# Performance work log

Measured on AMD Instinct MI355X. Metric: run time of the kernel, lower is better.

Reference implementation:

```python
import jax, jax.numpy as jnp
import numpy as np

B, T, C, H = 4, 2048, 1024, 16
DK = C // H


def setup_inputs() -> dict:
    key = jax.random.key(0)
    ks = jax.random.split(key, 12)
    s = 1.0 / np.sqrt(C)
    return {
        "q": jax.random.normal(ks[0], (B, T, C), jnp.float32),
        "k": jax.random.normal(ks[1], (B, T, C), jnp.float32),
        "v": jax.random.normal(ks[2], (B, T, C), jnp.float32),
        "mask": jax.random.randint(ks[3], (B, T, T), 0, 2, jnp.int32),
        "Wq": jax.random.normal(ks[4], (C, C), jnp.float32) * s,
        "bq": jnp.zeros((C,), jnp.float32),
        "Wk": jax.random.normal(ks[5], (C, C), jnp.float32) * s,
        "bk": jnp.zeros((C,), jnp.float32),
        "Wv": jax.random.normal(ks[6], (C, C), jnp.float32) * s,
        "bv": jnp.zeros((C,), jnp.float32),
        "Wf": jax.random.normal(ks[7], (C, C), jnp.float32) * s,
        "bf": jnp.zeros((C,), jnp.float32),
    }


def reference(q, k, v, mask, Wq, bq, Wk, bk, Wv, bv, Wf, bf):
    # linear projections (torch Linear: x @ W.T + b), then split heads
    def heads(x, W, b):
        y = x @ W.T + b  # [B,T,C]
        return y.reshape(B, T, H, DK).transpose(0, 2, 1, 3)  # [B,H,T,DK]

    qh, kh, vh = heads(q, Wq, bq), heads(k, Wk, bk), heads(v, Wv, bv)
    att = jnp.einsum("bhqd,bhkd->bhqk", qh, kh) * (1.0 / np.sqrt(DK))
    att = jnp.where(mask[:, None, :, :] == 0, jnp.float32(-1e9), att)
    p = jax.nn.softmax(att, axis=-1)
    y = jnp.einsum("bhqk,bhkd->bhqd", p, vh)  # [B,H,T,DK]
    y = y.transpose(0, 2, 1, 3).reshape(B, T, C)
    return y @ Wf.T + bf
```

## Files before the change

kernel.cpp:

```cpp
#include <hip/hip_runtime.h>

#define B_ 4
#define T_ 2048
#define C_ 1024
#define H_ 16
#define DK_ 64
#define BT_ 8192

using u16 = unsigned short;
using u32 = unsigned int;
using u64 = unsigned long long;
typedef __attribute__((ext_vector_type(8))) short short8;
typedef __attribute__((ext_vector_type(4))) float f32x4;
typedef __attribute__((ext_vector_type(16))) float f32x16;
typedef __attribute__((ext_vector_type(4))) u32 u32x4;
typedef __attribute__((ext_vector_type(2))) u32 u32x2;

__device__ __forceinline__ u16 f2bf(float f) {
  u32 u = __builtin_bit_cast(u32, f);
  u32 r = u + 0x7fffu + ((u >> 16) & 1u);
  return (u16)(r >> 16);
}

__device__ __forceinline__ void glds16(void* lds, const void* g) {
  __builtin_amdgcn_global_load_lds(
      (__attribute__((address_space(1))) u32*)g,
      (__attribute__((address_space(3))) u32*)lds, 16, 0, 0);
}

__device__ __forceinline__ u32 cvtpk_bf16(float lo, float hi) {
  u32 r;
  asm("v_cvt_pk_bf16_f32 %0, %1, %2" : "=v"(r) : "v"(lo), "v"(hi));
  return r;
}

__device__ __forceinline__ void cvt_range(const float* __restrict__ s,
                                          u16* __restrict__ d, int n,
                                          int rb, int nblk) {
  int i0 = (rb * 256 + (int)threadIdx.x) * 4;
  int stride = nblk * 256 * 4;
  for (int i = i0; i < n; i += stride) {
    float4 v = *(const float4*)(s + i);
    u64 p = (u64)f2bf(v.x) | ((u64)f2bf(v.y) << 16) |
            ((u64)f2bf(v.z) << 32) | ((u64)f2bf(v.w) << 48);
    *(u64*)(d + i) = p;
  }
}

__global__ __launch_bounds__(256) void prep_k(
    const float* __restrict__ q, const float* __restrict__ k,
    const float* __restrict__ v, const float* __restrict__ Wq,
    const float* __restrict__ Wk, const float* __restrict__ Wv,
    const float* __restrict__ Wf, const int* __restrict__ mask,
    u16* __restrict__ qb, u16* __restrict__ kb, u16* __restrict__ vb,
    u16* __restrict__ Wqb, u16* __restrict__ Wkb, u16* __restrict__ Wvb,
    u16* __restrict__ Wfb, u64* __restrict__ mb) {
  const int bid = blockIdx.x;
  if (bid < 1260) {
    const int which = bid / 420, rb = bid % 420;
    const float* s = which == 0 ? q : which == 1 ? k : v;
    u16* d = which == 0 ? qb : which == 1 ? kb : vb;
    cvt_range(s, d, BT_ * C_, rb, 420);
  } else if (bid < 1468) {
    const int which = (bid - 1260) / 52, rb = (bid - 1260) % 52;
    const float* s = which == 0 ? Wq : which == 1 ? Wk : which == 2 ? Wv : Wf;
    u16* d = which == 0 ? Wqb : which == 1 ? Wkb : which == 2 ? Wvb : Wfb;
    cvt_range(s, d, C_ * C_, rb, 52);
  } else {
    const int nch = B_ * T_ * T_ / 256;
    const int lane = threadIdx.x & 63;
    int g0 = (bid - 1468) * 16 + ((int)threadIdx.x >> 6) * 4;
    for (int g = g0; g < nch; g += 580 * 16) {
#pragma unroll
      for (int gg = 0; gg < 4; ++gg) {
        const int4 vv = *(const int4*)(mask + (size_t)(g + gg) * 256 + 4 * lane);
        const u64 b0 = __ballot(vv.x != 0);
        const u64 b1 = __ballot(vv.y != 0);
        const u64 b2 = __ballot(vv.z != 0);
        const u64 b3 = __ballot(vv.w != 0);
        const u64 wv = lane == 0 ? b0 : lane == 1 ? b1 : lane == 2 ? b2 : b3;
        if (lane < 4) mb[(size_t)(g + gg) * 4 + lane] = wv;
      }
    }
  }
}

template <int MODE>
__global__ __launch_bounds__(256) void gemm_nt(
    const u16* __restrict__ A, const u16* __restrict__ Bmat,
    const float* __restrict__ bias, void* __restrict__ out,
    int M, int N, int K, float scale) {
  __shared__ __align__(16) u16 As[128 * 32];
  __shared__ __align__(16) u16 Bs[128 * 32];
  const int t = threadIdx.x;
  const int lane = t & 63;
  const int wave = t >> 6;
  const int wr = wave >> 1, wc = wave & 1;
  const int lr = lane & 15, lg = lane >> 4;
  const int m0 = blockIdx.x * 128;
  const int n0 = blockIdx.y * 128;

  f32x4 acc[4][4] = {};

  const int srow = t >> 2;
  const int scol = (t & 3) * 8;
  const u16* ag = A + (size_t)(m0 + srow) * K + scol;
  const u16* bg = Bmat + (size_t)(n0 + srow) * K + scol;
  u16* as0 = &As[srow * 32 + scol];
  u16* as1 = &As[(srow + 64) * 32 + scol];
  u16* bs0 = &Bs[srow * 32 + scol];
  u16* bs1 = &Bs[(srow + 64) * 32 + scol];

  for (int k0 = 0; k0 < K; k0 += 32) {
    glds16(as0, ag + k0);
    glds16(as1, ag + (size_t)64 * K + k0);
    glds16(bs0, bg + k0);
    glds16(bs1, bg + (size_t)64 * K + k0);
    __syncthreads();
    short8 af[4], bf[4];
#pragma unroll
    for (int m = 0; m < 4; ++m)
      af[m] = *(const short8*)&As[(wr * 64 + m * 16 + lr) * 32 + lg * 8];
#pragma unroll
    for (int n = 0; n < 4; ++n)
      bf[n] = *(const short8*)&Bs[(wc * 64 + n * 16 + lr) * 32 + lg * 8];
#pragma unroll
    for (int m = 0; m < 4; ++m)
#pragma unroll
      for (int n = 0; n < 4; ++n)
        acc[m][n] = __builtin_amdgcn_mfma_f32_16x16x32_bf16(af[m], bf[n], acc[m][n], 0, 0, 0);
    __syncthreads();
  }

#pragma unroll
  for (int m = 0; m < 4; ++m) {
#pragma unroll
    for (int n = 0; n < 4; ++n) {
#pragma unroll
      for (int j = 0; j < 4; ++j) {
        const int gm = m0 + wr * 64 + m * 16 + lg * 4 + j;
        const int gn = n0 + wc * 64 + n * 16 + lr;
        float v = acc[m][n][j];
        if (MODE == 0) {
          v = (v + bias[gn]) * scale;
          const int b = gm >> 11, tt = gm & 2047, h = gn >> 6, d = gn & 63;
          ((u16*)out)[((((size_t)b * H_ + h) * T_ + tt) << 6) + d] = f2bf(v);
        } else if (MODE == 1) {
          v += bias[gm];
          const int gnp = (gn & ~12) | ((gn & 4) << 1) | ((gn & 8) >> 1);
          ((u16*)out)[(size_t)gm * N + gnp] = f2bf(v);
        } else {
          v += bias[gn];
          ((float*)out)[(size_t)gm * N + gn] = v;
        }
      }
    }
  }
}

__global__ __launch_bounds__(512) void attn32_k(
    const u16* __restrict__ Qh, const u16* __restrict__ Kh,
    const u16* __restrict__ Vt, const u64* __restrict__ mb,
    u16* __restrict__ Y) {
  __shared__ __align__(16) u16 Ks[2][64 * 68];
  __shared__ __align__(16) u16 Vs[2][64 * 68];

  const int f = blockIdx.x;
  const int lgid = ((f & 7) << 6) | (f >> 3);
  const int bh = lgid >> 3, qblk = lgid & 7;
  const int b = bh >> 4, h = bh & 15;
  const int t = threadIdx.x;
  const int wave = t >> 6, lane = t & 63;
  const int lq = lane & 31, hi = lane >> 5;
  const int q0 = qblk * 256 + wave * 32;

  const u16* Qp = Qh + ((size_t)bh * T_ + q0 + lq) * DK_ + hi * 8;
  short8 qf[4];
#pragma unroll
  for (int kt = 0; kt < 4; ++kt) qf[kt] = *(const short8*)(Qp + kt * 16);

  const u16* KgB = Kh + (size_t)bh * T_ * DK_;
  const u16* VtB = Vt + (size_t)h * DK_ * BT_ + (size_t)b * T_;
  const u64* mrow = mb + ((size_t)b * T_ + q0 + lq) * (T_ / 64);

  const int sr = t >> 3, sj = t & 7;
  const u16* ksrc0 = KgB + (size_t)sr * DK_ + sj * 8;
  const u16* vsrc0 = VtB + (size_t)sr * BT_ + sj * 8;
  const int ldst = sr * 68 + sj * 8;

  const u32x4 onesu = {0x3F803F80u, 0x3F803F80u, 0x3F803F80u, 0x3F803F80u};
  const short8 ones8 = __builtin_bit_cast(short8, onesu);

  f32x16 o0 = {}, o1 = {}, accl = {};

  u32x4 kpre = *(const u32x4*)(ksrc0);
  u32x4 vpre = *(const u32x4*)(vsrc0);
  *(u32x2*)&Ks[0][ldst] = (u32x2){kpre[0], kpre[1]};
  *(u32x2*)&Ks[0][ldst + 4] = (u32x2){kpre[2], kpre[3]};
  *(u32x2*)&Vs[0][ldst] = (u32x2){vpre[0], vpre[1]};
  *(u32x2*)&Vs[0][ldst + 4] = (u32x2){vpre[2], vpre[3]};
  __syncthreads();
  int cur = 0;

  for (int kv = 0; kv < T_; kv += 64) {
    const bool pre = (kv + 64) < T_;
    if (pre) {
      kpre = *(const u32x4*)(ksrc0 + (size_t)(kv + 64) * DK_);
      vpre = *(const u32x4*)(vsrc0 + (kv + 64));
    }

    f32x16 c0 = {}, c1 = {};
    __builtin_amdgcn_s_setprio(1);
#pragma unroll
    for (int kt = 0; kt < 4; ++kt) {
      const int ix = (2 * kt + hi) * 8;
      const u32x2 a0 = *(const u32x2*)&Ks[cur][lq * 68 + ix];
      const u32x2 a1 = *(const u32x2*)&Ks[cur][lq * 68 + ix + 4];
      const u32x2 b0 = *(const u32x2*)&Ks[cur][(lq + 32) * 68 + ix];
      const u32x2 b1 = *(const u32x2*)&Ks[cur][(lq + 32) * 68 + ix + 4];
      const u32x4 k0u = {a0[0], a0[1], a1[0], a1[1]};
      const u32x4 k1u = {b0[0], b0[1], b1[0], b1[1]};
      c0 = __builtin_amdgcn_mfma_f32_32x32x16_bf16(
          __builtin_bit_cast(short8, k0u), qf[kt], c0, 0, 0, 0);
      c1 = __builtin_amdgcn_mfma_f32_32x32x16_bf16(
          __builtin_bit_cast(short8, k1u), qf[kt], c1, 0, 0, 0);
    }
    __builtin_amdgcn_s_setprio(0);

    const u64* wp = mrow + ((kv >> 8) << 2);
    const int sh = ((kv >> 2) & 48) + hi;
    u32 tp[4];
#pragma unroll
    for (int e = 0; e < 4; ++e) tp[e] = (u32)(wp[e] >> sh);
#pragma unroll
    for (int r = 0; r < 16; ++r) {
      const int pp = 2 * (r >> 2);
      const u32 k0m = (u32)(((int)(tp[r & 3] << (31 - pp))) >> 31);
      const u32 k1m = (u32)(((int)(tp[r & 3] << (23 - pp))) >> 31);
      c0[r] = __builtin_bit_cast(
          float, __builtin_bit_cast(u32, __builtin_amdgcn_exp2f(c0[r])) & k0m);
      c1[r] = __builtin_bit_cast(
          float, __builtin_bit_cast(u32, __builtin_amdgcn_exp2f(c1[r])) & k1m);
    }

    u32 pw_[4][4];
#pragma unroll
    for (int g = 0; g < 4; ++g) {
      const int ob = (g & 1) * 8;
#pragma unroll
      for (int w2 = 0; w2 < 4; ++w2) {
        const float lo = (g < 2) ? c0[ob + 2 * w2] : c1[ob + 2 * w2];
        const float hii = (g < 2) ? c0[ob + 2 * w2 + 1] : c1[ob + 2 * w2 + 1];
        pw_[g][w2] = cvtpk_bf16(lo, hii);
      }
    }

    __builtin_amdgcn_s_setprio(1);
#pragma unroll
    for (int g = 0; g < 4; ++g) {
      const int ix = (2 * g + hi) * 8;
      const u32x2 va = *(const u32x2*)&Vs[cur][lq * 68 + ix];
      const u32x2 vb = *(const u32x2*)&Vs[cur][lq * 68 + ix + 4];
      const u32x2 wa = *(const u32x2*)&Vs[cur][(lq + 32) * 68 + ix];
      const u32x2 wb = *(const u32x2*)&Vs[cur][(lq + 32) * 68 + ix + 4];
      const u32x4 pu = {pw_[g][0], pw_[g][1], pw_[g][2], pw_[g][3]};
      const u32x4 v0u = {va[0], va[1], vb[0], vb[1]};
      const u32x4 v1u = {wa[0], wa[1], wb[0], wb[1]};
      const short8 pa = __builtin_bit_cast(short8, pu);
      o0 = __builtin_amdgcn_mfma_f32_32x32x16_bf16(
          pa, __builtin_bit_cast(short8, v0u), o0, 0, 0, 0);
      o1 = __builtin_amdgcn_mfma_f32_32x32x16_bf16(
          pa, __builtin_bit_cast(short8, v1u), o1, 0, 0, 0);
      accl = __builtin_amdgcn_mfma_f32_32x32x16_bf16(pa, ones8, accl, 0, 0, 0);
    }
    __builtin_amdgcn_s_setprio(0);

    if (pre) {
      *(u32x2*)&Ks[cur ^ 1][ldst] = (u32x2){kpre[0], kpre[1]};
      *(u32x2*)&Ks[cur ^ 1][ldst + 4] = (u32x2){kpre[2], kpre[3]};
      *(u32x2*)&Vs[cur ^ 1][ldst] = (u32x2){vpre[0], vpre[1]};
      *(u32x2*)&Vs[cur ^ 1][ldst + 4] = (u32x2){vpre[2], vpre[3]};
    }
    __syncthreads();
    cur ^= 1;
  }

#pragma unroll
  for (int r = 0; r < 16; ++r) {
    const int row = (r & 3) + 8 * (r >> 2) + 4 * hi;
    const float li = 1.0f / accl[r];
    u16* yp = Y + ((size_t)b * T_ + q0 + row) * C_ + h * DK_ + lq;
    yp[0] = f2bf(o0[r] * li);
    yp[32] = f2bf(o1[r] * li);
  }
}

extern "C" void kernel_launch(void* const* d_in, const int* in_sizes, int n_in,
                              void* d_out, int out_size, void* d_ws, size_t ws_size,
                              hipStream_t stream) {
  const float* q  = (const float*)d_in[0];
  const float* k  = (const float*)d_in[1];
  const float* v  = (const float*)d_in[2];
  const int* mask = (const int*)d_in[3];
  const float* Wq = (const float*)d_in[4];
  const float* bq = (const float*)d_in[5];
  const float* Wk = (const float*)d_in[6];
  const float* bk = (const float*)d_in[7];
  const float* Wv = (const float*)d_in[8];
  const float* bv = (const float*)d_in[9];
  const float* Wf = (const float*)d_in[10];
  const float* bf = (const float*)d_in[11];
  float* out = (float*)d_out;
  char* ws = (char*)d_ws;

  size_t off = 0;
  auto nxt = [&](size_t bytes) -> void* {
    void* p = ws + off;
    off += (bytes + 255) & ~(size_t)255;
    return p;
  };
  const size_t big = (size_t)BT_ * C_ * 2;
  const size_t wsz = (size_t)C_ * C_ * 2;
  u16* qb  = (u16*)nxt(big);
  u16* kb  = (u16*)nxt(big);
  u16* vb  = (u16*)nxt(big);
  u16* Wqb = (u16*)nxt(wsz);
  u16* Wkb = (u16*)nxt(wsz);
  u16* Wvb = (u16*)nxt(wsz);
  u16* Wfb = (u16*)nxt(wsz);
  u16* Qh  = (u16*)nxt(big);
  u16* Kh  = (u16*)nxt(big);
  u16* Vt  = (u16*)nxt(big);
  u16* Yb  = (u16*)nxt(big);
  u64* mb  = (u64*)nxt((size_t)B_ * T_ * (T_ / 64) * 8);

  prep_k<<<2048, 256, 0, stream>>>(q, k, v, Wq, Wk, Wv, Wf, mask,
                                   qb, kb, vb, Wqb, Wkb, Wvb, Wfb, mb);

  const float qscale = 0.125f * 1.4426950408889634f;
  gemm_nt<0><<<dim3(BT_ / 128, C_ / 128), 256, 0, stream>>>(qb, Wqb, bq, Qh, BT_, C_, C_, qscale);
  gemm_nt<0><<<dim3(BT_ / 128, C_ / 128), 256, 0, stream>>>(kb, Wkb, bk, Kh, BT_, C_, C_, 1.0f);
  gemm_nt<1><<<dim3(C_ / 128, BT_ / 128), 256, 0, stream>>>(Wvb, vb, bv, Vt, C_, BT_, C_, 1.0f);

  attn32_k<<<B_ * H_ * (T_ / 256), 512, 0, stream>>>(Qh, Kh, Vt, mb, Yb);

  gemm_nt<2><<<dim3(BT_ / 128, C_ / 128), 256, 0, stream>>>(Yb, Wfb, bf, out, BT_, C_, C_, 1.0f);
}
```

Baseline: 266.7 us.

## Fuse fp32-to-bf16 activation conversion into projection GEMMs and widen attention KV tile

The separate prep pass that converted q, k and v to bf16 is removed. The projection GEMMs now load fp32 activations directly, convert them in registers and store bf16 into LDS, with a register prefetch one k-step ahead. The Q and K projections are batched into a single launch through blockIdx.z. The attention kernel now stages 128 keys per LDS buffer and processes them as two 64-key sub-steps, halving the number of barriers and global prefetch rounds at the cost of more LDS and registers. Folding the conversion into the GEMMs cuts a full write and reread of bf16 activations, but the fp32 A operand doubles the GEMM's global load bytes.

Result: slower. 278.1 us (+4.3%).

```diff
diff --git a/kernel.cpp b/kernel.cpp
--- a/kernel.cpp
+++ b/kernel.cpp
@@ -48,29 +48,22 @@
 }
 
 __global__ __launch_bounds__(256) void prep_k(
-    const float* __restrict__ q, const float* __restrict__ k,
-    const float* __restrict__ v, const float* __restrict__ Wq,
-    const float* __restrict__ Wk, const float* __restrict__ Wv,
-    const float* __restrict__ Wf, const int* __restrict__ mask,
-    u16* __restrict__ qb, u16* __restrict__ kb, u16* __restrict__ vb,
+    const float* __restrict__ Wq, const float* __restrict__ Wk,
+    const float* __restrict__ Wv, const float* __restrict__ Wf,
+    const int* __restrict__ mask,
     u16* __restrict__ Wqb, u16* __restrict__ Wkb, u16* __restrict__ Wvb,
     u16* __restrict__ Wfb, u64* __restrict__ mb) {
   const int bid = blockIdx.x;
-  if (bid < 1260) {
-    const int which = bid / 420, rb = bid % 420;
-    const float* s = which == 0 ? q : which == 1 ? k : v;
-    u16* d = which == 0 ? qb : which == 1 ? kb : vb;
-    cvt_range(s, d, BT_ * C_, rb, 420);
-  } else if (bid < 1468) {
-    const int which = (bid - 1260) / 52, rb = (bid - 1260) % 52;
+  if (bid < 256) {
+    const int which = bid >> 6, rb = bid & 63;
     const float* s = which == 0 ? Wq : which == 1 ? Wk : which == 2 ? Wv : Wf;
     u16* d = which == 0 ? Wqb : which == 1 ? Wkb : which == 2 ? Wvb : Wfb;
-    cvt_range(s, d, C_ * C_, rb, 52);
+    cvt_range(s, d, C_ * C_, rb, 64);
   } else {
     const int nch = B_ * T_ * T_ / 256;
     const int lane = threadIdx.x & 63;
-    int g0 = (bid - 1468) * 16 + ((int)threadIdx.x >> 6) * 4;
-    for (int g = g0; g < nch; g += 580 * 16) {
+    int g0 = (bid - 256) * 16 + ((int)threadIdx.x >> 6) * 4;
+    for (int g = g0; g < nch; g += 1792 * 16) {
 #pragma unroll
       for (int gg = 0; gg < 4; ++gg) {
         const int4 vv = *(const int4*)(mask + (size_t)(g + gg) * 256 + 4 * lane);
@@ -85,13 +78,21 @@
   }
 }
 
-template <int MODE>
+template <int MODE, int AF, int BF>
 __global__ __launch_bounds__(256) void gemm_nt(
-    const u16* __restrict__ A, const u16* __restrict__ Bmat,
-    const float* __restrict__ bias, void* __restrict__ out,
-    int M, int N, int K, float scale) {
+    const void* __restrict__ Aa, const void* __restrict__ Ab,
+    const void* __restrict__ Ba, const void* __restrict__ Bb,
+    const float* __restrict__ biasa, const float* __restrict__ biasb,
+    void* __restrict__ outa, void* __restrict__ outb,
+    int M, int N, int K, float scalea, float scaleb) {
   __shared__ __align__(16) u16 As[128 * 32];
   __shared__ __align__(16) u16 Bs[128 * 32];
+  const void* A = blockIdx.z ? Ab : Aa;
+  const void* Bm = blockIdx.z ? Bb : Ba;
+  const float* bias = blockIdx.z ? biasb : biasa;
+  void* out = blockIdx.z ? outb : outa;
+  const float scale = blockIdx.z ? scaleb : scalea;
+
   const int t = threadIdx.x;
   const int lane = t & 63;
   const int wave = t >> 6;
@@ -104,18 +105,65 @@
 
   const int srow = t >> 2;
   const int scol = (t & 3) * 8;
-  const u16* ag = A + (size_t)(m0 + srow) * K + scol;
-  const u16* bg = Bmat + (size_t)(n0 + srow) * K + scol;
   u16* as0 = &As[srow * 32 + scol];
   u16* as1 = &As[(srow + 64) * 32 + scol];
   u16* bs0 = &Bs[srow * 32 + scol];
   u16* bs1 = &Bs[(srow + 64) * 32 + scol];
 
+  const u16* ag = (const u16*)A + (size_t)(m0 + srow) * K + scol;
+  const float* agf = (const float*)A + (size_t)(m0 + srow) * K + scol;
+  const u16* bg = (const u16*)Bm + (size_t)(n0 + srow) * K + scol;
+  const float* bgf = (const float*)Bm + (size_t)(n0 + srow) * K + scol;
+
+  float4 ax0, ax1, ax2, ax3, bx0, bx1, bx2, bx3;
+  if (AF) {
+    ax0 = *(const float4*)(agf);
+    ax1 = *(const float4*)(agf + 4);
+    ax2 = *(const float4*)(agf + (size_t)64 * K);
+    ax3 = *(const float4*)(agf + (size_t)64 * K + 4);
+  }
+  if (BF) {
+    bx0 = *(const float4*)(bgf);
+    bx1 = *(const float4*)(bgf + 4);
+    bx2 = *(const float4*)(bgf + (size_t)64 * K);
+    bx3 = *(const float4*)(bgf + (size_t)64 * K + 4);
+  }
+
   for (int k0 = 0; k0 < K; k0 += 32) {
-    glds16(as0, ag + k0);
-    glds16(as1, ag + (size_t)64 * K + k0);
-    glds16(bs0, bg + k0);
-    glds16(bs1, bg + (size_t)64 * K + k0);
+    if (AF) {
+      const u32x4 p0 = {cvtpk_bf16(ax0.x, ax0.y), cvtpk_bf16(ax0.z, ax0.w),
+                        cvtpk_bf16(ax1.x, ax1.y), cvtpk_bf16(ax1.z, ax1.w)};
+      const u32x4 p1 = {cvtpk_bf16(ax2.x, ax2.y), cvtpk_bf16(ax2.z, ax2.w),
+                        cvtpk_bf16(ax3.x, ax3.y), cvtpk_bf16(ax3.z, ax3.w)};
+      *(u32x4*)as0 = p0;
+      *(u32x4*)as1 = p1;
+      if (k0 + 32 < K) {
+        ax0 = *(const float4*)(agf + k0 + 32);
+        ax1 = *(const float4*)(agf + k0 + 36);
+        ax2 = *(const float4*)(agf + (size_t)64 * K + k0 + 32);
+        ax3 = *(const float4*)(agf + (size_t)64 * K + k0 + 36);
+      }
+    } else {
+      glds16(as0, ag + k0);
+      glds16(as1, ag + (size_t)64 * K + k0);
+    }
+    if (BF) {
+      const u32x4 p0 = {cvtpk_bf16(bx0.x, bx0.y), cvtpk_bf16(bx0.z, bx0.w),
+                        cvtpk_bf16(bx1.x, bx1.y), cvtpk_bf16(bx1.z, bx1.w)};
+      const u32x4 p1 = {cvtpk_bf16(bx2.x, bx2.y), cvtpk_bf16(bx2.z, bx2.w),
+                        cvtpk_bf16(bx3.x, bx3.y), cvtpk_bf16(bx3.z, bx3.w)};
+      *(u32x4*)bs0 = p0;
+      *(u32x4*)bs1 = p1;
+      if (k0 + 32 < K) {
+        bx0 = *(const float4*)(bgf + k0 + 32);
+        bx1 = *(const float4*)(bgf + k0 + 36);
+        bx2 = *(const float4*)(bgf + (size_t)64 * K + k0 + 32);
+        bx3 = *(const float4*)(bgf + (size_t)64 * K + k0 + 36);
+      }
+    } else {
+      glds16(bs0, bg + k0);
+      glds16(bs1, bg + (size_t)64 * K + k0);
+    }
     __syncthreads();
     short8 af[4], bf[4];
 #pragma unroll
@@ -162,8 +210,8 @@
     const u16* __restrict__ Qh, const u16* __restrict__ Kh,
     const u16* __restrict__ Vt, const u64* __restrict__ mb,
     u16* __restrict__ Y) {
-  __shared__ __align__(16) u16 Ks[2][64 * 68];
-  __shared__ __align__(16) u16 Vs[2][64 * 68];
+  __shared__ __align__(16) u16 Ks[2][128 * 68];
+  __shared__ __align__(16) u16 Vs[2][64 * 132];
 
   const int f = blockIdx.x;
   const int lgid = ((f & 7) << 6) | (f >> 3);
@@ -183,103 +231,121 @@
   const u16* VtB = Vt + (size_t)h * DK_ * BT_ + (size_t)b * T_;
   const u64* mrow = mb + ((size_t)b * T_ + q0 + lq) * (T_ / 64);
 
-  const int sr = t >> 3, sj = t & 7;
-  const u16* ksrc0 = KgB + (size_t)sr * DK_ + sj * 8;
-  const u16* vsrc0 = VtB + (size_t)sr * BT_ + sj * 8;
-  const int ldst = sr * 68 + sj * 8;
+  const int kr = t >> 3, ku = t & 7;
+  const u16* ksrcA = KgB + (size_t)kr * DK_ + ku * 8;
+  const u16* ksrcB = KgB + (size_t)(kr + 64) * DK_ + ku * 8;
+  const int kdstA = kr * 68 + ku * 8, kdstB = (kr + 64) * 68 + ku * 8;
+  const int vr = t >> 4, vu = t & 15;
+  const u16* vsrcA = VtB + (size_t)vr * BT_ + vu * 8;
+  const u16* vsrcB = VtB + (size_t)(vr + 32) * BT_ + vu * 8;
+  const int vdstA = vr * 132 + vu * 8, vdstB = (vr + 32) * 132 + vu * 8;
 
   const u32x4 onesu = {0x3F803F80u, 0x3F803F80u, 0x3F803F80u, 0x3F803F80u};
   const short8 ones8 = __builtin_bit_cast(short8, onesu);
 
   f32x16 o0 = {}, o1 = {}, accl = {};
 
-  u32x4 kpre = *(const u32x4*)(ksrc0);
-  u32x4 vpre = *(const u32x4*)(vsrc0);
-  *(u32x2*)&Ks[0][ldst] = (u32x2){kpre[0], kpre[1]};
-  *(u32x2*)&Ks[0][ldst + 4] = (u32x2){kpre[2], kpre[3]};
-  *(u32x2*)&Vs[0][ldst] = (u32x2){vpre[0], vpre[1]};
-  *(u32x2*)&Vs[0][ldst + 4] = (u32x2){vpre[2], vpre[3]};
+  u32x4 kpA = *(const u32x4*)(ksrcA), kpB = *(const u32x4*)(ksrcB);
+  u32x4 vpA = *(const u32x4*)(vsrcA), vpB = *(const u32x4*)(vsrcB);
+  *(u32x2*)&Ks[0][kdstA] = (u32x2){kpA[0], kpA[1]};
+  *(u32x2*)&Ks[0][kdstA + 4] = (u32x2){kpA[2], kpA[3]};
+  *(u32x2*)&Ks[0][kdstB] = (u32x2){kpB[0], kpB[1]};
+  *(u32x2*)&Ks[0][kdstB + 4] = (u32x2){kpB[2], kpB[3]};
+  *(u32x2*)&Vs[0][vdstA] = (u32x2){vpA[0], vpA[1]};
+  *(u32x2*)&Vs[0][vdstA + 4] = (u32x2){vpA[2], vpA[3]};
+  *(u32x2*)&Vs[0][vdstB] = (u32x2){vpB[0], vpB[1]};
+  *(u32x2*)&Vs[0][vdstB + 4] = (u32x2){vpB[2], vpB[3]};
   __syncthreads();
   int cur = 0;
 
-  for (int kv = 0; kv < T_; kv += 64) {
-    const bool pre = (kv + 64) < T_;
+  for (int kv = 0; kv < T_; kv += 128) {
+    const bool pre = (kv + 128) < T_;
     if (pre) {
-      kpre = *(const u32x4*)(ksrc0 + (size_t)(kv + 64) * DK_);
-      vpre = *(const u32x4*)(vsrc0 + (kv + 64));
-    }
-
-    f32x16 c0 = {}, c1 = {};
-    __builtin_amdgcn_s_setprio(1);
-#pragma unroll
-    for (int kt = 0; kt < 4; ++kt) {
-      const int ix = (2 * kt + hi) * 8;
-      const u32x2 a0 = *(const u32x2*)&Ks[cur][lq * 68 + ix];
-      const u32x2 a1 = *(const u32x2*)&Ks[cur][lq * 68 + ix + 4];
-      const u32x2 b0 = *(const u32x2*)&Ks[cur][(lq + 32) * 68 + ix];
-      const u32x2 b1 = *(const u32x2*)&Ks[cur][(lq + 32) * 68 + ix + 4];
-      const u32x4 k0u = {a0[0], a0[1], a1[0], a1[1]};
-      const u32x4 k1u = {b0[0], b0[1], b1[0], b1[1]};
-      c0 = __builtin_amdgcn_mfma_f32_32x32x16_bf16(
-          __builtin_bit_cast(short8, k0u), qf[kt], c0, 0, 0, 0);
-      c1 = __builtin_amdgcn_mfma_f32_32x32x16_bf16(
-          __builtin_bit_cast(short8, k1u), qf[kt], c1, 0, 0, 0);
-    }
-    __builtin_amdgcn_s_setprio(0);
-
-    const u64* wp = mrow + ((kv >> 8) << 2);
-    const int sh = ((kv >> 2) & 48) + hi;
-    u32 tp[4];
-#pragma unroll
-    for (int e = 0; e < 4; ++e) tp[e] = (u32)(wp[e] >> sh);
-#pragma unroll
-    for (int r = 0; r < 16; ++r) {
-      const int pp = 2 * (r >> 2);
-      const u32 k0m = (u32)(((int)(tp[r & 3] << (31 - pp))) >> 31);
-      const u32 k1m = (u32)(((int)(tp[r & 3] << (23 - pp))) >> 31);
-      c0[r] = __builtin_bit_cast(
-          float, __builtin_bit_cast(u32, __builtin_amdgcn_exp2f(c0[r])) & k0m);
-      c1[r] = __builtin_bit_cast(
-          float, __builtin_bit_cast(u32, __builtin_amdgcn_exp2f(c1[r])) & k1m);
-    }
-
-    u32 pw_[4][4];
-#pragma unroll
-    for (int g = 0; g < 4; ++g) {
-      const int ob = (g & 1) * 8;
-#pragma unroll
-      for (int w2 = 0; w2 < 4; ++w2) {
-        const float lo = (g < 2) ? c0[ob + 2 * w2] : c1[ob + 2 * w2];
-        const float hii = (g < 2) ? c0[ob + 2 * w2 + 1] : c1[ob + 2 * w2 + 1];
-        pw_[g][w2] = cvtpk_bf16(lo, hii);
-      }
-    }
-
-    __builtin_amdgcn_s_setprio(1);
-#pragma unroll
-    for (int g = 0; g < 4; ++g) {
-      const int ix = (2 * g + hi) * 8;
-      const u32x2 va = *(const u32x2*)&Vs[cur][lq * 68 + ix];
-      const u32x2 vb = *(const u32x2*)&Vs[cur][lq * 68 + ix + 4];
-      const u32x2 wa = *(const u32x2*)&Vs[cur][(lq + 32) * 68 + ix];
-      const u32x2 wb = *(const u32x2*)&Vs[cur][(lq + 32) * 68 + ix + 4];
-      const u32x4 pu = {pw_[g][0], pw_[g][1], pw_[g][2], pw_[g][3]};
-      const u32x4 v0u = {va[0], va[1], vb[0], vb[1]};
-      const u32x4 v1u = {wa[0], wa[1], wb[0], wb[1]};
-      const short8 pa = __builtin_bit_cast(short8, pu);
-      o0 = __builtin_amdgcn_mfma_f32_32x32x16_bf16(
-          pa, __builtin_bit_cast(short8, v0u), o0, 0, 0, 0);
-      o1 = __builtin_amdgcn_mfma_f32_32x32x16_bf16(
-          pa, __builtin_bit_cast(short8, v1u), o1, 0, 0, 0);
-      accl = __builtin_amdgcn_mfma_f32_32x32x16_bf16(pa, ones8, accl, 0, 0, 0);
-    }
-    __builtin_amdgcn_s_setprio(0);
+      kpA = *(const u32x4*)(ksrcA + (size_t)(kv + 128) * DK_);
+      kpB = *(const u32x4*)(ksrcB + (size_t)(kv + 128) * DK_);
+      vpA = *(const u32x4*)(vsrcA + (kv + 128));
+      vpB = *(const u32x4*)(vsrcB + (kv + 128));
+    }
+
+#pragma unroll
+    for (int s2 = 0; s2 < 2; ++s2) {
+      const int kvs = kv + 64 * s2;
+      f32x16 c0 = {}, c1 = {};
+      __builtin_amdgcn_s_setprio(1);
+#pragma unroll
+      for (int kt = 0; kt < 4; ++kt) {
+        const int ix = (2 * kt + hi) * 8;
+        const u32x2 a0 = *(const u32x2*)&Ks[cur][(64 * s2 + lq) * 68 + ix];
+        const u32x2 a1 = *(const u32x2*)&Ks[cur][(64 * s2 + lq) * 68 + ix + 4];
+        const u32x2 b0 = *(const u32x2*)&Ks[cur][(64 * s2 + lq + 32) * 68 + ix];
+        const u32x2 b1 = *(const u32x2*)&Ks[cur][(64 * s2 + lq + 32) * 68 + ix + 4];
+        const u32x4 k0u = {a0[0], a0[1], a1[0], a1[1]};
+        const u32x4 k1u = {b0[0], b0[1], b1[0], b1[1]};
+        c0 = __builtin_amdgcn_mfma_f32_32x32x16_bf16(
+            __builtin_bit_cast(short8, k0u), qf[kt], c0, 0, 0, 0);
+        c1 = __builtin_amdgcn_mfma_f32_32x32x16_bf16(
+            __builtin_bit_cast(short8, k1u), qf[kt], c1, 0, 0, 0);
+      }
+      __builtin_amdgcn_s_setprio(0);
+
+      const u64* wp = mrow + ((kvs >> 8) << 2);
+      const int sh = ((kvs >> 2) & 48) + hi;
+      u32 tp[4];
+#pragma unroll
+      for (int e = 0; e < 4; ++e) tp[e] = (u32)(wp[e] >> sh);
+#pragma unroll
+      for (int r = 0; r < 16; ++r) {
+        const int pp = 2 * (r >> 2);
+        const u32 k0m = (u32)(((int)(tp[r & 3] << (31 - pp))) >> 31);
+        const u32 k1m = (u32)(((int)(tp[r & 3] << (23 - pp))) >> 31);
+        c0[r] = __builtin_bit_cast(
+            float, __builtin_bit_cast(u32, __builtin_amdgcn_exp2f(c0[r])) & k0m);
+        c1[r] = __builtin_bit_cast(
+            float, __builtin_bit_cast(u32, __builtin_amdgcn_exp2f(c1[r])) & k1m);
+      }
+
+      u32 pw_[4][4];
+#pragma unroll
+      for (int g = 0; g < 4; ++g) {
+        const int ob = (g & 1) * 8;
+#pragma unroll
+        for (int w2 = 0; w2 < 4; ++w2) {
+          const float lo = (g < 2) ? c0[ob + 2 * w2] : c1[ob + 2 * w2];
+          const float hii = (g < 2) ? c0[ob + 2 * w2 + 1] : c1[ob + 2 * w2 + 1];
+          pw_[g][w2] = cvtpk_bf16(lo, hii);
+        }
+      }
+
+      __builtin_amdgcn_s_setprio(1);
+#pragma unroll
+      for (int g = 0; g < 4; ++g) {
+        const int ix = 16 * (4 * s2 + g) + 8 * hi;
+        const u32x2 va = *(const u32x2*)&Vs[cur][lq * 132 + ix];
+        const u32x2 vb = *(const u32x2*)&Vs[cur][lq * 132 + ix + 4];
+        const u32x2 wa = *(const u32x2*)&Vs[cur][(lq + 32) * 132 + ix];
+        const u32x2 wb = *(const u32x2*)&Vs[cur][(lq + 32) * 132 + ix + 4];
+        const u32x4 pu = {pw_[g][0], pw_[g][1], pw_[g][2], pw_[g][3]};
+        const u32x4 v0u = {va[0], va[1], vb[0], vb[1]};
+        const u32x4 v1u = {wa[0], wa[1], wb[0], wb[1]};
+        const short8 pa = __builtin_bit_cast(short8, pu);
+        o0 = __builtin_amdgcn_mfma_f32_32x32x16_bf16(
+            pa, __builtin_bit_cast(short8, v0u), o0, 0, 0, 0);
+        o1 = __builtin_amdgcn_mfma_f32_32x32x16_bf16(
+            pa, __builtin_bit_cast(short8, v1u), o1, 0, 0, 0);
+        accl = __builtin_amdgcn_mfma_f32_32x32x16_bf16(pa, ones8, accl, 0, 0, 0);
+      }
+      __builtin_amdgcn_s_setprio(0);
+    }
 
     if (pre) {
-      *(u32x2*)&Ks[cur ^ 1][ldst] = (u32x2){kpre[0], kpre[1]};
-      *(u32x2*)&Ks[cur ^ 1][ldst + 4] = (u32x2){kpre[2], kpre[3]};
-      *(u32x2*)&Vs[cur ^ 1][ldst] = (u32x2){vpre[0], vpre[1]};
-      *(u32x2*)&Vs[cur ^ 1][ldst + 4] = (u32x2){vpre[2], vpre[3]};
+      *(u32x2*)&Ks[cur ^ 1][kdstA] = (u32x2){kpA[0], kpA[1]};
+      *(u32x2*)&Ks[cur ^ 1][kdstA + 4] = (u32x2){kpA[2], kpA[3]};
+      *(u32x2*)&Ks[cur ^ 1][kdstB] = (u32x2){kpB[0], kpB[1]};
+      *(u32x2*)&Ks[cur ^ 1][kdstB + 4] = (u32x2){kpB[2], kpB[3]};
+      *(u32x2*)&Vs[cur ^ 1][vdstA] = (u32x2){vpA[0], vpA[1]};
+      *(u32x2*)&Vs[cur ^ 1][vdstA + 4] = (u32x2){vpA[2], vpA[3]};
+      *(u32x2*)&Vs[cur ^ 1][vdstB] = (u32x2){vpB[0], vpB[1]};
+      *(u32x2*)&Vs[cur ^ 1][vdstB + 4] = (u32x2){vpB[2], vpB[3]};
     }
     __syncthreads();
     cur ^= 1;
@@ -321,9 +387,6 @@
   };
   const size_t big = (size_t)BT_ * C_ * 2;
   const size_t wsz = (size_t)C_ * C_ * 2;
-  u16* qb  = (u16*)nxt(big);
-  u16* kb  = (u16*)nxt(big);
-  u16* vb  = (u16*)nxt(big);
   u16* Wqb = (u16*)nxt(wsz);
   u16* Wkb = (u16*)nxt(wsz);
   u16* Wvb = (u16*)nxt(wsz);
@@ -334,15 +397,17 @@
   u16* Yb  = (u16*)nxt(big);
   u64* mb  = (u64*)nxt((size_t)B_ * T_ * (T_ / 64) * 8);
 
-  prep_k<<<2048, 256, 0, stream>>>(q, k, v, Wq, Wk, Wv, Wf, mask,
-                                   qb, kb, vb, Wqb, Wkb, Wvb, Wfb, mb);
+  prep_k<<<2048, 256, 0, stream>>>(Wq, Wk, Wv, Wf, mask,
+                                   Wqb, Wkb, Wvb, Wfb, mb);
 
   const float qscale = 0.125f * 1.4426950408889634f;
-  gemm_nt<0><<<dim3(BT_ / 128, C_ / 128), 256, 0, stream>>>(qb, Wqb, bq, Qh, BT_, C_, C_, qscale);
-  gemm_nt<0><<<dim3(BT_ / 128, C_ / 128), 256, 0, stream>>>(kb, Wkb, bk, Kh, BT_, C_, C_, 1.0f);
-  gemm_nt<1><<<dim3(C_ / 128, BT_ / 128), 256, 0, stream>>>(Wvb, vb, bv, Vt, C_, BT_, C_, 1.0f);
+  gemm_nt<0, 1, 0><<<dim3(BT_ / 128, C_ / 128, 2), 256, 0, stream>>>(
+      q, k, Wqb, Wkb, bq, bk, Qh, Kh, BT_, C_, C_, qscale, 1.0f);
+  gemm_nt<1, 0, 1><<<dim3(C_ / 128, BT_ / 128, 1), 256, 0, stream>>>(
+      Wvb, Wvb, v, v, bv, bv, Vt, Vt, C_, BT_, C_, 1.0f, 1.0f);
 
   attn32_k<<<B_ * H_ * (T_ / 256), 512, 0, stream>>>(Qh, Kh, Vt, mb, Yb);
 
-  gemm_nt<2><<<dim3(BT_ / 128, C_ / 128), 256, 0, stream>>>(Yb, Wfb, bf, out, BT_, C_, C_, 1.0f);
-}
+  gemm_nt<2, 0, 0><<<dim3(BT_ / 128, C_ / 128, 1), 256, 0, stream>>>(
+      Yb, Yb, Wfb, Wfb, bf, bf, out, out, BT_, C_, C_, 1.0f, 1.0f);
+}
```

## Stage K/V via direct global-to-LDS loads with XOR swizzle and 128-key tiles

Applied to the files above, without the earlier changes.

Replaces the register-staged K/V prefetch (global load into registers, then padded LDS stores) with direct global-to-LDS loads (glds16), using an XOR-swizzled unpadded layout. The KV tile grows from 64 to 128 keys per barrier, halving the number of __syncthreads and letting each fragment be read as one 16-byte LDS load. This removes register pressure and VGPR round trips from staging. It doubles LDS use per block, which may reduce occupancy, and relies on glds16 completion being ordered by the barrier.

Result: no change. 265.5 us (-0.5%).

```diff
diff --git a/kernel.cpp b/kernel.cpp
--- a/kernel.cpp
+++ b/kernel.cpp
@@ -162,8 +162,8 @@
     const u16* __restrict__ Qh, const u16* __restrict__ Kh,
     const u16* __restrict__ Vt, const u64* __restrict__ mb,
     u16* __restrict__ Y) {
-  __shared__ __align__(16) u16 Ks[2][64 * 68];
-  __shared__ __align__(16) u16 Vs[2][64 * 68];
+  __shared__ __align__(16) u16 Ks[2][128 * 64];
+  __shared__ __align__(16) u16 Vs[2][64 * 128];
 
   const int f = blockIdx.x;
   const int lgid = ((f & 7) << 6) | (f >> 3);
@@ -183,104 +183,89 @@
   const u16* VtB = Vt + (size_t)h * DK_ * BT_ + (size_t)b * T_;
   const u64* mrow = mb + ((size_t)b * T_ + q0 + lq) * (T_ / 64);
 
-  const int sr = t >> 3, sj = t & 7;
-  const u16* ksrc0 = KgB + (size_t)sr * DK_ + sj * 8;
-  const u16* vsrc0 = VtB + (size_t)sr * BT_ + sj * 8;
-  const int ldst = sr * 68 + sj * 8;
+  auto stage = [&](int buf, int kv) {
+#pragma unroll
+    for (int s = 0; s < 2; ++s) {
+      const int c = t + s * 512;
+      const int kr2 = c >> 3, ku2 = c & 7;
+      glds16(&Ks[buf][c * 8],
+             KgB + (size_t)(kv + kr2) * DK_ + ((ku2 ^ (kr2 & 7)) << 3));
+      const int vr2 = c >> 4, vu2 = c & 15;
+      glds16(&Vs[buf][c * 8],
+             VtB + (size_t)vr2 * BT_ + kv + ((vu2 ^ (vr2 & 7)) << 3));
+    }
+  };
 
   const u32x4 onesu = {0x3F803F80u, 0x3F803F80u, 0x3F803F80u, 0x3F803F80u};
   const short8 ones8 = __builtin_bit_cast(short8, onesu);
 
   f32x16 o0 = {}, o1 = {}, accl = {};
 
-  u32x4 kpre = *(const u32x4*)(ksrc0);
-  u32x4 vpre = *(const u32x4*)(vsrc0);
-  *(u32x2*)&Ks[0][ldst] = (u32x2){kpre[0], kpre[1]};
-  *(u32x2*)&Ks[0][ldst + 4] = (u32x2){kpre[2], kpre[3]};
-  *(u32x2*)&Vs[0][ldst] = (u32x2){vpre[0], vpre[1]};
-  *(u32x2*)&Vs[0][ldst + 4] = (u32x2){vpre[2], vpre[3]};
+  stage(0, 0);
   __syncthreads();
   int cur = 0;
 
-  for (int kv = 0; kv < T_; kv += 64) {
-    const bool pre = (kv + 64) < T_;
-    if (pre) {
-      kpre = *(const u32x4*)(ksrc0 + (size_t)(kv + 64) * DK_);
-      vpre = *(const u32x4*)(vsrc0 + (kv + 64));
+  for (int kv = 0; kv < T_; kv += 128) {
+    if (kv + 128 < T_) stage(cur ^ 1, kv + 128);
+
+#pragma unroll
+    for (int s2 = 0; s2 < 2; ++s2) {
+      const int kvs = kv + 64 * s2;
+      f32x16 c0 = {}, c1 = {};
+      __builtin_amdgcn_s_setprio(1);
+#pragma unroll
+      for (int kt = 0; kt < 4; ++kt) {
+        const int u = (2 * kt + hi) ^ (lq & 7);
+        const short8 k0 = *(const short8*)&Ks[cur][(64 * s2 + lq) * 64 + u * 8];
+        const short8 k1 = *(const short8*)&Ks[cur][(64 * s2 + lq + 32) * 64 + u * 8];
+        c0 = __builtin_amdgcn_mfma_f32_32x32x16_bf16(k0, qf[kt], c0, 0, 0, 0);
+        c1 = __builtin_amdgcn_mfma_f32_32x32x16_bf16(k1, qf[kt], c1, 0, 0, 0);
+      }
+      __builtin_amdgcn_s_setprio(0);
+
+      const u64* wp = mrow + ((kvs >> 8) << 2);
+      const int sh = ((kvs >> 2) & 48) + hi;
+      u32 tp[4];
+#pragma unroll
+      for (int e = 0; e < 4; ++e) tp[e] = (u32)(wp[e] >> sh);
+#pragma unroll
+      for (int r = 0; r < 16; ++r) {
+        const int pp = 2 * (r >> 2);
+        const u32 k0m = (u32)(((int)(tp[r & 3] << (31 - pp))) >> 31);
+        const u32 k1m = (u32)(((int)(tp[r & 3] << (23 - pp))) >> 31);
+        c0[r] = __builtin_bit_cast(
+            float, __builtin_bit_cast(u32, __builtin_amdgcn_exp2f(c0[r])) & k0m);
+        c1[r] = __builtin_bit_cast(
+            float, __builtin_bit_cast(u32, __builtin_amdgcn_exp2f(c1[r])) & k1m);
+      }
+
+      u32 pw_[4][4];
+#pragma unroll
+      for (int g = 0; g < 4; ++g) {
+        const int ob = (g & 1) * 8;
+#pragma unroll
+        for (int w2 = 0; w2 < 4; ++w2) {
+          const float lo = (g < 2) ? c0[ob + 2 * w2] : c1[ob + 2 * w2];
+          const float hii = (g < 2) ? c0[ob + 2 * w2 + 1] : c1[ob + 2 * w2 + 1];
+          pw_[g][w2] = cvtpk_bf16(lo, hii);
+        }
+      }
+
+      __builtin_amdgcn_s_setprio(1);
+#pragma unroll
+      for (int g = 0; g < 4; ++g) {
+        const int u = (2 * (4 * s2 + g) + hi) ^ (lq & 7);
+        const short8 v0 = *(const short8*)&Vs[cur][lq * 128 + u * 8];
+        const short8 v1 = *(const short8*)&Vs[cur][(lq + 32) * 128 + u * 8];
+        const u32x4 pu = {pw_[g][0], pw_[g][1], pw_[g][2], pw_[g][3]};
+        const short8 pa = __builtin_bit_cast(short8, pu);
+        o0 = __builtin_amdgcn_mfma_f32_32x32x16_bf16(pa, v0, o0, 0, 0, 0);
+        o1 = __builtin_amdgcn_mfma_f32_32x32x16_bf16(pa, v1, o1, 0, 0, 0);
+        accl = __builtin_amdgcn_mfma_f32_32x32x16_bf16(pa, ones8, accl, 0, 0, 0);
+      }
+      __builtin_amdgcn_s_setprio(0);
     }
 
-    f32x16 c0 = {}, c1 = {};
-    __builtin_amdgcn_s_setprio(1);
-#pragma unroll
-    for (int kt = 0; kt < 4; ++kt) {
-      const int ix = (2 * kt + hi) * 8;
-      const u32x2 a0 = *(const u32x2*)&Ks[cur][lq * 68 + ix];
-      const u32x2 a1 = *(const u32x2*)&Ks[cur][lq * 68 + ix + 4];
-      const u32x2 b0 = *(const u32x2*)&Ks[cur][(lq + 32) * 68 + ix];
-      const u32x2 b1 = *(const u32x2*)&Ks[cur][(lq + 32) * 68 + ix + 4];
-      const u32x4 k0u = {a0[0], a0[1], a1[0], a1[1]};
-      const u32x4 k1u = {b0[0], b0[1], b1[0], b1[1]};
-      c0 = __builtin_amdgcn_mfma_f32_32x32x16_bf16(
-          __builtin_bit_cast(short8, k0u), qf[kt], c0, 0, 0, 0);
-      c1 = __builtin_amdgcn_mfma_f32_32x32x16_bf16(
-          __builtin_bit_cast(short8, k1u), qf[kt], c1, 0, 0, 0);
-    }
-    __builtin_amdgcn_s_setprio(0);
-
-    const u64* wp = mrow + ((kv >> 8) << 2);
-    const int sh = ((kv >> 2) & 48) + hi;
-    u32 tp[4];
-#pragma unroll
-    for (int e = 0; e < 4; ++e) tp[e] = (u32)(wp[e] >> sh);
-#pragma unroll
-    for (int r = 0; r < 16; ++r) {
-      const int pp = 2 * (r >> 2);
-      const u32 k0m = (u32)(((int)(tp[r & 3] << (31 - pp))) >> 31);
-      const u32 k1m = (u32)(((int)(tp[r & 3] << (23 - pp))) >> 31);
-      c0[r] = __builtin_bit_cast(
-          float, __builtin_bit_cast(u32, __builtin_amdgcn_exp2f(c0[r])) & k0m);
-      c1[r] = __builtin_bit_cast(
-          float, __builtin_bit_cast(u32, __builtin_amdgcn_exp2f(c1[r])) & k1m);
-    }
-
-    u32 pw_[4][4];
-#pragma unroll
-    for (int g = 0; g < 4; ++g) {
-      const int ob = (g & 1) * 8;
-#pragma unroll
-      for (int w2 = 0; w2 < 4; ++w2) {
-        const float lo = (g < 2) ? c0[ob + 2 * w2] : c1[ob + 2 * w2];
-        const float hii = (g < 2) ? c0[ob + 2 * w2 + 1] : c1[ob + 2 * w2 + 1];
-        pw_[g][w2] = cvtpk_bf16(lo, hii);
-      }
-    }
-
-    __builtin_amdgcn_s_setprio(1);
-#pragma unroll
-    for (int g = 0; g < 4; ++g) {
-      const int ix = (2 * g + hi) * 8;
-      const u32x2 va = *(const u32x2*)&Vs[cur][lq * 68 + ix];
-      const u32x2 vb = *(const u32x2*)&Vs[cur][lq * 68 + ix + 4];
-      const u32x2 wa = *(const u32x2*)&Vs[cur][(lq + 32) * 68 + ix];
-      const u32x2 wb = *(const u32x2*)&Vs[cur][(lq + 32) * 68 + ix + 4];
-      const u32x4 pu = {pw_[g][0], pw_[g][1], pw_[g][2], pw_[g][3]};
-      const u32x4 v0u = {va[0], va[1], vb[0], vb[1]};
-      const u32x4 v1u = {wa[0], wa[1], wb[0], wb[1]};
-      const short8 pa = __builtin_bit_cast(short8, pu);
-      o0 = __builtin_amdgcn_mfma_f32_32x32x16_bf16(
-          pa, __builtin_bit_cast(short8, v0u), o0, 0, 0, 0);
-      o1 = __builtin_amdgcn_mfma_f32_32x32x16_bf16(
-          pa, __builtin_bit_cast(short8, v1u), o1, 0, 0, 0);
-      accl = __builtin_amdgcn_mfma_f32_32x32x16_bf16(pa, ones8, accl, 0, 0, 0);
-    }
-    __builtin_amdgcn_s_setprio(0);
-
-    if (pre) {
-      *(u32x2*)&Ks[cur ^ 1][ldst] = (u32x2){kpre[0], kpre[1]};
-      *(u32x2*)&Ks[cur ^ 1][ldst + 4] = (u32x2){kpre[2], kpre[3]};
-      *(u32x2*)&Vs[cur ^ 1][ldst] = (u32x2){vpre[0], vpre[1]};
-      *(u32x2*)&Vs[cur ^ 1][ldst + 4] = (u32x2){vpre[2], vpre[3]};
-    }
     __syncthreads();
     cur ^= 1;
   }
```
